# Optimization experiments

Measured on AMD Instinct MI355X. Metric: run time of the kernel, lower is better.

## Reference

```python
import jax, jax.numpy as jnp
import numpy as np

B, L, E, H = 2, 2048, 1024, 16
D = E // H  # head dim = 64


def setup_inputs() -> dict:
    key = jax.random.key(0)
    ks = jax.random.split(key, 10)
    s = 0.02
    return {
        "xt": jax.random.normal(ks[0], (B, L, E), jnp.float32),
        "xs": jax.random.normal(ks[1], (B, L, E), jnp.float32),
        "Wt": jax.random.normal(ks[2], (E, 3 * E), jnp.float32) * s,  # t_attn weight (x @ Wt)
        "bt": jnp.zeros((3 * E,), jnp.float32),
        "Ws": jax.random.normal(ks[3], (E, 2 * E), jnp.float32) * s,  # s_attn weight
        "bs": jnp.zeros((2 * E,), jnp.float32),
        "Wc": jax.random.normal(ks[4], (E, E), jnp.float32) * s,      # c_proj weight
        "bc": jnp.zeros((E,), jnp.float32),
        "lam_ts": jnp.ones((1,), jnp.float32),
        "lam_st": jnp.ones((1,), jnp.float32),
        "lam_ss": jnp.ones((1,), jnp.float32),
    }


def _heads(x):
    # (B, L, E) -> (B, H, L, D)
    return x.reshape(B, L, H, D).transpose(0, 2, 1, 3)


def reference(xt, xs, Wt, bt, Ws, bs, Wc, bc, lam_ts, lam_st, lam_ss):
    qt, kt, vt = jnp.split(xt @ Wt + bt, 3, axis=2)
    qs, ks = jnp.split(xs @ Ws + bs, 2, axis=2)
    qt, kt, vt, qs, ks = map(_heads, (qt, kt, vt, qs, ks))

    # 4-way disentangled scores; fuse the 4 matmuls into 2 by combining keys:
    # qt@kt^T + lam_ts*qt@ks^T = qt @ (kt + lam_ts*ks)^T
    # lam_st*qs@kt^T + lam_ss*qs@ks^T = qs @ (lam_st*kt + lam_ss*ks)^T
    k1 = kt + lam_ts[0] * ks
    k2 = lam_st[0] * kt + lam_ss[0] * ks
    att = (jnp.einsum('bhqd,bhkd->bhqk', qt, k1)
           + jnp.einsum('bhqd,bhkd->bhqk', qs, k2)) * (1.0 / np.sqrt(D))
    att = jax.nn.softmax(att, axis=-1)
    y = jnp.einsum('bhqk,bhkd->bhqd', att, vt)  # (B, H, L, D)
    y = y.transpose(0, 2, 1, 3).reshape(B, L, E)
    return y @ Wc + bc
```

## Files before the change

kernel.cpp:

```cpp
#include <hip/hip_runtime.h>
#include <math.h>

#define LQ 2048
#define EQ 1024
#define M_ROWS 4096
#define BH 32

typedef _Float16 f16x8 __attribute__((ext_vector_type(8)));
typedef _Float16 f16x4 __attribute__((ext_vector_type(4)));
typedef _Float16 f16x2 __attribute__((ext_vector_type(2)));
typedef float f32x4 __attribute__((ext_vector_type(4)));
typedef float f32x16 __attribute__((ext_vector_type(16)));

#define QSCALE 0.1803368801111204f

__device__ __forceinline__ void async_ld16(const _Float16* g, _Float16* l) {
  __builtin_amdgcn_global_load_lds(
      (const __attribute__((address_space(1))) unsigned int*)g,
      (__attribute__((address_space(3))) unsigned int*)l, 16, 0, 0);
}

__global__ __launch_bounds__(256) void prep(
    const float* __restrict__ xt, const float* __restrict__ xs,
    const float* __restrict__ Wt, const float* __restrict__ Ws,
    const float* __restrict__ Wc,
    _Float16* __restrict__ xt16, _Float16* __restrict__ xs16,
    _Float16* __restrict__ WtT, _Float16* __restrict__ WsT,
    _Float16* __restrict__ WcT) {
  int gb = blockIdx.x;
  if (gb < 4096) {
    int i = gb * 256 + threadIdx.x;
    const float* s; _Float16* d; size_t off;
    if (i < 524288) { s = xt; d = xt16; off = (size_t)i * 8; }
    else            { s = xs; d = xs16; off = (size_t)(i - 524288) * 8; }
    float4 a = *(const float4*)&s[off];
    float4 b = *(const float4*)&s[off + 4];
    f16x8 h;
    h[0] = (_Float16)a.x; h[1] = (_Float16)a.y; h[2] = (_Float16)a.z; h[3] = (_Float16)a.w;
    h[4] = (_Float16)b.x; h[5] = (_Float16)b.y; h[6] = (_Float16)b.z; h[7] = (_Float16)b.w;
    *(f16x8*)&d[off] = h;
  } else {
    __shared__ float T[32][33];
    int tb = gb - 4096;
    int tx = threadIdx.x & 31, ty = threadIdx.x >> 5;
    int c0 = (tb % 192) * 32;
    int k0 = (tb / 192) * 32;
    const float* W; _Float16* D; int Nw, cl;
    if (c0 < 3072)      { W = Wt; D = WtT; Nw = 3072; cl = c0; }
    else if (c0 < 5120) { W = Ws; D = WsT; Nw = 2048; cl = c0 - 3072; }
    else                { W = Wc; D = WcT; Nw = 1024; cl = c0 - 5120; }
#pragma unroll
    for (int j = 0; j < 4; ++j)
      T[ty + j * 8][tx] = W[(size_t)(k0 + ty + j * 8) * Nw + cl + tx];
    __syncthreads();
#pragma unroll
    for (int j = 0; j < 4; ++j)
      D[(size_t)(cl + ty + j * 8) * 1024 + k0 + tx] = (_Float16)T[tx][ty + j * 8];
  }
}

__global__ __launch_bounds__(256) void proj_gemm(
    const _Float16* __restrict__ xt16, const _Float16* __restrict__ xs16,
    const _Float16* __restrict__ WtT, const _Float16* __restrict__ WsT,
    const float* __restrict__ bt, const float* __restrict__ bs,
    _Float16* __restrict__ q16, _Float16* __restrict__ k16,
    _Float16* __restrict__ v16) {
  __shared__ _Float16 Al[128 * 32];
  __shared__ _Float16 Bl[128 * 32];

  const int tid = threadIdx.x;
  const int w = tid >> 6;
  const int lane = tid & 63;
  const int quad = lane >> 4;
  const int l15 = lane & 15;
  const int wm = w >> 1, wn = w & 1;
  const int by = blockIdx.y;
  const int n0 = blockIdx.x * 128;

  const _Float16* Ab;
  const _Float16* Bb;
  const float* bias;
  int m0, bsel = 0, branch;
  if (by < 32) {
    branch = 0; Ab = xt16; Bb = WtT; bias = bt; m0 = by * 128;
  } else if (by < 48) {
    branch = 1;
    int by2 = by - 32;
    bsel = by2 >> 3;
    m0 = (by2 & 7) * 128;
    Ab = WtT + (size_t)2048 * 1024;
    Bb = xt16 + (size_t)bsel * 2048 * 1024;
    bias = bt;
  } else {
    branch = 2; Ab = xs16; Bb = WsT; bias = bs; m0 = (by - 48) * 128;
  }

  const int srow = lane >> 2;
  const int schunk = ((lane & 3) ^ ((lane >> 3) & 3)) * 8;

  f32x4 acc[4][4];
#pragma unroll
  for (int mb = 0; mb < 4; ++mb)
#pragma unroll
    for (int nb = 0; nb < 4; ++nb) acc[mb][nb] = (f32x4){0.f, 0.f, 0.f, 0.f};

  const int key = (l15 >> 1) & 3;

  for (int kt = 0; kt < 1024; kt += 32) {
    __syncthreads();
#pragma unroll
    for (int i = 0; i < 2; ++i) {
      int rt = w * 32 + i * 16;
      async_ld16(&Ab[(size_t)(m0 + rt + srow) * 1024 + kt + schunk], &Al[rt * 32]);
      async_ld16(&Bb[(size_t)(n0 + rt + srow) * 1024 + kt + schunk], &Bl[rt * 32]);
    }
    __syncthreads();

    f16x8 af[4], bf[4];
    const int pc = (quad ^ key) * 8;
#pragma unroll
    for (int mb = 0; mb < 4; ++mb)
      af[mb] = *(f16x8*)&Al[(wm * 64 + mb * 16 + l15) * 32 + pc];
#pragma unroll
    for (int nb = 0; nb < 4; ++nb)
      bf[nb] = *(f16x8*)&Bl[(wn * 64 + nb * 16 + l15) * 32 + pc];
#pragma unroll
    for (int mb = 0; mb < 4; ++mb)
#pragma unroll
      for (int nb = 0; nb < 4; ++nb)
        acc[mb][nb] = __builtin_amdgcn_mfma_f32_16x16x32_f16(af[mb], bf[nb], acc[mb][nb], 0, 0, 0);
  }

#pragma unroll
  for (int mb = 0; mb < 4; ++mb)
#pragma unroll
    for (int nb = 0; nb < 4; ++nb)
#pragma unroll
      for (int r = 0; r < 4; ++r) {
        int row = m0 + wm * 64 + mb * 16 + quad * 4 + r;
        int col = n0 + wn * 64 + nb * 16 + l15;
        if (branch == 1) {
          float val = acc[mb][nb][r] + bias[2048 + row];
          v16[(size_t)(bsel * 1024 + row) * 2048 + col] = (_Float16)val;
        } else {
          float val = acc[mb][nb][r] + bias[col];
          int bb = row >> 11, ll = row & 2047;
          int which = col >> 10, e = col & 1023;
          int hh = e >> 6, dd = e & 63;
          size_t rowhd = (size_t)(bb * 16 + hh) * 2048 + ll;
          int off = (branch == 0) ? 0 : 64;
          if (which == 0) q16[rowhd * 128 + off + dd] = (_Float16)val;
          else            k16[rowhd * 128 + off + dd] = (_Float16)val;
        }
      }
}

__global__ __launch_bounds__(256) void cproj_gemm(
    const _Float16* __restrict__ A, const _Float16* __restrict__ Bm,
    const float* __restrict__ bias, float* __restrict__ outf) {
  __shared__ _Float16 Al[128 * 32];
  __shared__ _Float16 Bl[128 * 32];

  const int tid = threadIdx.x;
  const int w = tid >> 6;
  const int lane = tid & 63;
  const int quad = lane >> 4;
  const int l15 = lane & 15;
  const int wm = w >> 1, wn = w & 1;
  const int m0 = blockIdx.y * 128;
  const int n0 = blockIdx.x * 128;

  const int srow = lane >> 2;
  const int schunk = ((lane & 3) ^ ((lane >> 3) & 3)) * 8;

  f32x4 acc[4][4];
#pragma unroll
  for (int mb = 0; mb < 4; ++mb)
#pragma unroll
    for (int nb = 0; nb < 4; ++nb) acc[mb][nb] = (f32x4){0.f, 0.f, 0.f, 0.f};

  const int key = (l15 >> 1) & 3;

  for (int kt = 0; kt < 1024; kt += 32) {
    __syncthreads();
#pragma unroll
    for (int i = 0; i < 2; ++i) {
      int rt = w * 32 + i * 16;
      async_ld16(&A[(size_t)(m0 + rt + srow) * 1024 + kt + schunk], &Al[rt * 32]);
      async_ld16(&Bm[(size_t)(n0 + rt + srow) * 1024 + kt + schunk], &Bl[rt * 32]);
    }
    __syncthreads();

    f16x8 af[4], bf[4];
    const int pc = (quad ^ key) * 8;
#pragma unroll
    for (int mb = 0; mb < 4; ++mb)
      af[mb] = *(f16x8*)&Al[(wm * 64 + mb * 16 + l15) * 32 + pc];
#pragma unroll
    for (int nb = 0; nb < 4; ++nb)
      bf[nb] = *(f16x8*)&Bl[(wn * 64 + nb * 16 + l15) * 32 + pc];
#pragma unroll
    for (int mb = 0; mb < 4; ++mb)
#pragma unroll
      for (int nb = 0; nb < 4; ++nb)
        acc[mb][nb] = __builtin_amdgcn_mfma_f32_16x16x32_f16(af[mb], bf[nb], acc[mb][nb], 0, 0, 0);
  }

#pragma unroll
  for (int mb = 0; mb < 4; ++mb)
#pragma unroll
    for (int nb = 0; nb < 4; ++nb)
#pragma unroll
      for (int r = 0; r < 4; ++r) {
        int row = m0 + wm * 64 + mb * 16 + quad * 4 + r;
        int col = n0 + wn * 64 + nb * 16 + l15;
        outf[(size_t)row * 1024 + col] = acc[mb][nb][r] + bias[col];
      }
}

__global__ __launch_bounds__(256, 2) void flash_attn_mfma(
    const _Float16* __restrict__ qcat, const _Float16* __restrict__ kcat,
    const _Float16* __restrict__ vT, _Float16* __restrict__ y,
    const float* __restrict__ lam_ts, const float* __restrict__ lam_st,
    const float* __restrict__ lam_ss) {
  const int bh = blockIdx.y;
  const int qt0 = blockIdx.x * 128;
  const int b = bh >> 4, h = bh & 15;
  const _Float16* Qg = qcat + (size_t)bh * LQ * 128;
  const _Float16* Kg = kcat + (size_t)bh * LQ * 128;
  const _Float16* Vg = vT + (size_t)bh * 64 * LQ;

  __shared__ _Float16 Ksh0[64 * 128];
  __shared__ _Float16 Ksh1[64 * 128];
  __shared__ _Float16 Vsh0[64 * 64];
  __shared__ _Float16 Vsh1[64 * 64];

  const int tid = threadIdx.x;
  const int w = tid >> 6;
  const int lane = tid & 63;
  const int half = lane >> 5;
  const int l31 = lane & 31;

  const float lts = lam_ts[0], lst = lam_st[0], lss = lam_ss[0];

  f16x8 qf[8];
#pragma unroll
  for (int db = 0; db < 4; ++db) {
    const _Float16* qp = &Qg[(size_t)(qt0 + w * 32 + l31) * 128 + db * 16 + half * 8];
    f16x8 a = *(const f16x8*)qp;
    f16x8 bq = *(const f16x8*)(qp + 64);
#pragma unroll
    for (int e = 0; e < 8; ++e) {
      float fa = (float)a[e], fb = (float)bq[e];
      qf[db][e]     = (_Float16)(QSCALE * (fa + lst * fb));
      qf[db + 4][e] = (_Float16)(QSCALE * (lts * fa + lss * fb));
    }
  }

  float m_i = -INFINITY;
  float l_i = 0.f;
  f32x16 O[2];
#pragma unroll
  for (int nt = 0; nt < 2; ++nt)
#pragma unroll
    for (int r = 0; r < 16; ++r) O[nt][r] = 0.f;

  auto dma = [&](int t, _Float16* Kd, _Float16* Vd) {
#pragma unroll
    for (int a = 0; a < 4; ++a) {
      int row = w * 16 + a * 4 + (lane >> 4);
      int sc = (lane & 15) ^ (row & 7);
      async_ld16(&Kg[(size_t)(t + row) * 128 + sc * 8], &Kd[(w * 16 + a * 4) * 128]);
    }
#pragma unroll
    for (int a = 0; a < 2; ++a) {
      int row = w * 16 + a * 8 + (lane >> 3);
      int sc = (lane & 7) ^ (row & 7);
      async_ld16(&Vg[(size_t)row * LQ + t + sc * 8], &Vd[(w * 16 + a * 8) * 64]);
    }
  };

  auto compute = [&](const _Float16* Ks, const _Float16* Vs) {
    f32x16 S[2];
#pragma unroll
    for (int kb = 0; kb < 2; ++kb)
#pragma unroll
      for (int r = 0; r < 16; ++r) S[kb][r] = 0.f;
#pragma unroll
    for (int db = 0; db < 8; ++db) {
      const int pc = ((db * 2 + half) ^ (lane & 7)) * 8;
      f16x8 af[2];
#pragma unroll
      for (int kb = 0; kb < 2; ++kb)
        af[kb] = *(const f16x8*)&Ks[(kb * 32 + l31) * 128 + pc];
#pragma unroll
      for (int kb = 0; kb < 2; ++kb)
        S[kb] = __builtin_amdgcn_mfma_f32_32x32x16_f16(af[kb], qf[db], S[kb], 0, 0, 0);
    }

    float mx = -INFINITY;
#pragma unroll
    for (int kb = 0; kb < 2; ++kb)
#pragma unroll
      for (int r = 0; r < 16; ++r) mx = fmaxf(mx, S[kb][r]);
    mx = fmaxf(mx, __shfl_xor(mx, 32));
    float m_new = fmaxf(m_i, mx);
    float alpha = __builtin_amdgcn_exp2f(m_i - m_new);
    float s = 0.f;
#pragma unroll
    for (int kb = 0; kb < 2; ++kb)
#pragma unroll
      for (int r = 0; r < 16; ++r) {
        float p = __builtin_amdgcn_exp2f(S[kb][r] - m_new);
        S[kb][r] = p;
        s += p;
      }
    s += __shfl_xor(s, 32);
    l_i = l_i * alpha + s;
    m_i = m_new;

#pragma unroll
    for (int nt = 0; nt < 2; ++nt)
#pragma unroll
      for (int r = 0; r < 16; ++r) O[nt][r] *= alpha;

    unsigned pu[2][8];
#pragma unroll
    for (int kb = 0; kb < 2; ++kb)
#pragma unroll
      for (int i = 0; i < 8; ++i) {
        f16x2 t2;
        t2[0] = (_Float16)S[kb][2 * i];
        t2[1] = (_Float16)S[kb][2 * i + 1];
        pu[kb][i] = __builtin_bit_cast(unsigned, t2);
      }

#pragma unroll
    for (int kb = 0; kb < 2; ++kb)
#pragma unroll
      for (int c = 0; c < 2; ++c) {
        unsigned ulo0 = pu[kb][4 * c + 0], ulo1 = pu[kb][4 * c + 1];
        unsigned uhi0 = pu[kb][4 * c + 2], uhi1 = pu[kb][4 * c + 3];
        unsigned rlo0 = (unsigned)__shfl_xor((int)ulo0, 32);
        unsigned rlo1 = (unsigned)__shfl_xor((int)ulo1, 32);
        unsigned rhi0 = (unsigned)__shfl_xor((int)uhi0, 32);
        unsigned rhi1 = (unsigned)__shfl_xor((int)uhi1, 32);
        union { unsigned u[4]; f16x8 v; } pb;
        pb.u[0] = half ? rhi0 : ulo0;
        pb.u[1] = half ? rhi1 : ulo1;
        pb.u[2] = half ? uhi0 : rlo0;
        pb.u[3] = half ? uhi1 : rlo1;
        int kb2 = kb * 2 + c;
        f16x8 av[2];
#pragma unroll
        for (int nt = 0; nt < 2; ++nt) {
          int dim = nt * 32 + l31;
          int pc = ((kb2 * 2 + half) ^ (dim & 7)) * 8;
          av[nt] = *(const f16x8*)&Vs[dim * 64 + pc];
        }
#pragma unroll
        for (int nt = 0; nt < 2; ++nt)
          O[nt] = __builtin_amdgcn_mfma_f32_32x32x16_f16(av[nt], pb.v, O[nt], 0, 0, 0);
      }
  };

  dma(0, Ksh0, Vsh0);
  for (int t = 0; t < LQ; t += 128) {
    __syncthreads();
    dma(t + 64, Ksh1, Vsh1);
    compute(Ksh0, Vsh0);
    __syncthreads();
    if (t + 128 < LQ) dma(t + 128, Ksh0, Vsh0);
    compute(Ksh1, Vsh1);
  }

  float inv = 1.f / l_i;
  int qrow = qt0 + w * 32 + l31;
#pragma unroll
  for (int nt = 0; nt < 2; ++nt)
#pragma unroll
    for (int rg = 0; rg < 4; ++rg) {
      f16x4 o4;
#pragma unroll
      for (int i = 0; i < 4; ++i) o4[i] = (_Float16)(O[nt][rg * 4 + i] * inv);
      int dim = nt * 32 + rg * 8 + half * 4;
      *(f16x4*)&y[((size_t)b * LQ + qrow) * EQ + h * 64 + dim] = o4;
    }
}

extern "C" void kernel_launch(void* const* d_in, const int* in_sizes, int n_in,
                              void* d_out, int out_size, void* d_ws, size_t ws_size,
                              hipStream_t stream) {
  const float* xt = (const float*)d_in[0];
  const float* xs = (const float*)d_in[1];
  const float* Wt = (const float*)d_in[2];
  const float* bt = (const float*)d_in[3];
  const float* Ws = (const float*)d_in[4];
  const float* bs = (const float*)d_in[5];
  const float* Wc = (const float*)d_in[6];
  const float* bc = (const float*)d_in[7];
  const float* lam_ts = (const float*)d_in[8];
  const float* lam_st = (const float*)d_in[9];
  const float* lam_ss = (const float*)d_in[10];
  float* out = (float*)d_out;

  _Float16* w16 = (_Float16*)d_ws;
  _Float16* xt16 = w16;
  _Float16* xs16 = xt16 + 4194304;
  _Float16* WtT  = xs16 + 4194304;
  _Float16* WsT  = WtT + 3145728;
  _Float16* WcT  = WsT + 2097152;
  _Float16* qcat = WcT + 1048576;
  _Float16* kcat = qcat + 8388608;
  _Float16* vbufT = kcat + 8388608;
  _Float16* ybuf = vbufT + 4194304;

  prep<<<10240, 256, 0, stream>>>(xt, xs, Wt, Ws, Wc, xt16, xs16, WtT, WsT, WcT);
  proj_gemm<<<dim3(16, 80), 256, 0, stream>>>(
      xt16, xs16, WtT, WsT, bt, bs, qcat, kcat, vbufT);
  flash_attn_mfma<<<dim3(16, 32), 256, 0, stream>>>(
      qcat, kcat, vbufT, ybuf, lam_ts, lam_st, lam_ss);
  cproj_gemm<<<dim3(8, 32), 256, 0, stream>>>(ybuf, WcT, bc, out);
}
```

Measured before the change: 281.9 us.

## Double-buffer LDS tiles in projection GEMMs and narrow c_proj N-tile

Both proj_gemm and cproj_gemm now use two LDS buffers. The async global-to-LDS loads for the next K-slice are issued before the MFMA work on the current slice, so load latency is meant to overlap compute instead of sitting between two barriers. cproj_gemm also shrinks its N tile from 128 to 64, which doubles the grid to 512 blocks for better CU coverage at the cost of more A-tile re-reads. The extra LDS buffers increase per-block shared memory use, which may lower occupancy.

```diff
diff --git a/kernel.cpp b/kernel.cpp
--- a/kernel.cpp
+++ b/kernel.cpp
@@ -65,8 +65,10 @@
     const float* __restrict__ bt, const float* __restrict__ bs,
     _Float16* __restrict__ q16, _Float16* __restrict__ k16,
     _Float16* __restrict__ v16) {
-  __shared__ _Float16 Al[128 * 32];
-  __shared__ _Float16 Bl[128 * 32];
+  __shared__ _Float16 Al0[128 * 32];
+  __shared__ _Float16 Bl0[128 * 32];
+  __shared__ _Float16 Al1[128 * 32];
+  __shared__ _Float16 Bl1[128 * 32];
 
   const int tid = threadIdx.x;
   const int w = tid >> 6;
@@ -106,29 +108,39 @@
 
   const int key = (l15 >> 1) & 3;
 
-  for (int kt = 0; kt < 1024; kt += 32) {
-    __syncthreads();
+  auto dma = [&](int kt, _Float16* Al, _Float16* Bl) {
 #pragma unroll
     for (int i = 0; i < 2; ++i) {
       int rt = w * 32 + i * 16;
       async_ld16(&Ab[(size_t)(m0 + rt + srow) * 1024 + kt + schunk], &Al[rt * 32]);
       async_ld16(&Bb[(size_t)(n0 + rt + srow) * 1024 + kt + schunk], &Bl[rt * 32]);
     }
-    __syncthreads();
-
+  };
+
+  auto comp = [&](const _Float16* Al, const _Float16* Bl) {
     f16x8 af[4], bf[4];
     const int pc = (quad ^ key) * 8;
 #pragma unroll
     for (int mb = 0; mb < 4; ++mb)
-      af[mb] = *(f16x8*)&Al[(wm * 64 + mb * 16 + l15) * 32 + pc];
+      af[mb] = *(const f16x8*)&Al[(wm * 64 + mb * 16 + l15) * 32 + pc];
 #pragma unroll
     for (int nb = 0; nb < 4; ++nb)
-      bf[nb] = *(f16x8*)&Bl[(wn * 64 + nb * 16 + l15) * 32 + pc];
+      bf[nb] = *(const f16x8*)&Bl[(wn * 64 + nb * 16 + l15) * 32 + pc];
 #pragma unroll
     for (int mb = 0; mb < 4; ++mb)
 #pragma unroll
       for (int nb = 0; nb < 4; ++nb)
         acc[mb][nb] = __builtin_amdgcn_mfma_f32_16x16x32_f16(af[mb], bf[nb], acc[mb][nb], 0, 0, 0);
+  };
+
+  dma(0, Al0, Bl0);
+  for (int kt = 0; kt < 1024; kt += 64) {
+    __syncthreads();
+    dma(kt + 32, Al1, Bl1);
+    comp(Al0, Bl0);
+    __syncthreads();
+    if (kt + 64 < 1024) dma(kt + 64, Al0, Bl0);
+    comp(Al1, Bl1);
   }
 
 #pragma unroll
@@ -158,8 +170,10 @@
 __global__ __launch_bounds__(256) void cproj_gemm(
     const _Float16* __restrict__ A, const _Float16* __restrict__ Bm,
     const float* __restrict__ bias, float* __restrict__ outf) {
-  __shared__ _Float16 Al[128 * 32];
-  __shared__ _Float16 Bl[128 * 32];
+  __shared__ _Float16 Al0[128 * 32];
+  __shared__ _Float16 Bl0[64 * 32];
+  __shared__ _Float16 Al1[128 * 32];
+  __shared__ _Float16 Bl1[64 * 32];
 
   const int tid = threadIdx.x;
   const int w = tid >> 6;
@@ -168,52 +182,63 @@
   const int l15 = lane & 15;
   const int wm = w >> 1, wn = w & 1;
   const int m0 = blockIdx.y * 128;
-  const int n0 = blockIdx.x * 128;
+  const int n0 = blockIdx.x * 64;
 
   const int srow = lane >> 2;
   const int schunk = ((lane & 3) ^ ((lane >> 3) & 3)) * 8;
 
-  f32x4 acc[4][4];
+  f32x4 acc[4][2];
 #pragma unroll
   for (int mb = 0; mb < 4; ++mb)
 #pragma unroll
-    for (int nb = 0; nb < 4; ++nb) acc[mb][nb] = (f32x4){0.f, 0.f, 0.f, 0.f};
+    for (int nb = 0; nb < 2; ++nb) acc[mb][nb] = (f32x4){0.f, 0.f, 0.f, 0.f};
 
   const int key = (l15 >> 1) & 3;
 
-  for (int kt = 0; kt < 1024; kt += 32) {
-    __syncthreads();
+  auto dma = [&](int kt, _Float16* Al, _Float16* Bl) {
 #pragma unroll
     for (int i = 0; i < 2; ++i) {
       int rt = w * 32 + i * 16;
       async_ld16(&A[(size_t)(m0 + rt + srow) * 1024 + kt + schunk], &Al[rt * 32]);
-      async_ld16(&Bm[(size_t)(n0 + rt + srow) * 1024 + kt + schunk], &Bl[rt * 32]);
-    }
-    __syncthreads();
-
-    f16x8 af[4], bf[4];
+    }
+    int rtb = w * 16;
+    async_ld16(&Bm[(size_t)(n0 + rtb + srow) * 1024 + kt + schunk], &Bl[rtb * 32]);
+  };
+
+  auto comp = [&](const _Float16* Al, const _Float16* Bl) {
+    f16x8 af[4], bf[2];
     const int pc = (quad ^ key) * 8;
 #pragma unroll
     for (int mb = 0; mb < 4; ++mb)
-      af[mb] = *(f16x8*)&Al[(wm * 64 + mb * 16 + l15) * 32 + pc];
-#pragma unroll
-    for (int nb = 0; nb < 4; ++nb)
-      bf[nb] = *(f16x8*)&Bl[(wn * 64 + nb * 16 + l15) * 32 + pc];
+      af[mb] = *(const f16x8*)&Al[(wm * 64 + mb * 16 + l15) * 32 + pc];
+#pragma unroll
+    for (int nb = 0; nb < 2; ++nb)
+      bf[nb] = *(const f16x8*)&Bl[(wn * 32 + nb * 16 + l15) * 32 + pc];
 #pragma unroll
     for (int mb = 0; mb < 4; ++mb)
 #pragma unroll
-      for (int nb = 0; nb < 4; ++nb)
+      for (int nb = 0; nb < 2; ++nb)
         acc[mb][nb] = __builtin_amdgcn_mfma_f32_16x16x32_f16(af[mb], bf[nb], acc[mb][nb], 0, 0, 0);
+  };
+
+  dma(0, Al0, Bl0);
+  for (int kt = 0; kt < 1024; kt += 64) {
+    __syncthreads();
+    dma(kt + 32, Al1, Bl1);
+    comp(Al0, Bl0);
+    __syncthreads();
+    if (kt + 64 < 1024) dma(kt + 64, Al0, Bl0);
+    comp(Al1, Bl1);
   }
 
 #pragma unroll
   for (int mb = 0; mb < 4; ++mb)
 #pragma unroll
-    for (int nb = 0; nb < 4; ++nb)
+    for (int nb = 0; nb < 2; ++nb)
 #pragma unroll
       for (int r = 0; r < 4; ++r) {
         int row = m0 + wm * 64 + mb * 16 + quad * 4 + r;
-        int col = n0 + wn * 64 + nb * 16 + l15;
+        int col = n0 + wn * 32 + nb * 16 + l15;
         outf[(size_t)row * 1024 + col] = acc[mb][nb][r] + bias[col];
       }
 }
@@ -420,5 +445,5 @@
       xt16, xs16, WtT, WsT, bt, bs, qcat, kcat, vbufT);
   flash_attn_mfma<<<dim3(16, 32), 256, 0, stream>>>(
       qcat, kcat, vbufT, ybuf, lam_ts, lam_st, lam_ss);
-  cproj_gemm<<<dim3(8, 32), 256, 0, stream>>>(ybuf, WcT, bc, out);
-}
+  cproj_gemm<<<dim3(16, 32), 256, 0, stream>>>(ybuf, WcT, bc, out);
+}
```

Measured after the change: 279.4 us. No clear change (-0.9%).
